# Performance work log

Hardware: AMD Instinct MI355X
Metric: run time of the kernel (lower is better)

Reference implementation:

```python
import jax, jax.numpy as jnp
import numpy as np

B, T, D, H, Q = 8, 1024, 256, 4, 3
DK = D // H


def _ln(x, g, b):
    m = x.mean(-1, keepdims=True)
    v = x.var(-1, keepdims=True)
    return (x - m) / jnp.sqrt(v + 1e-5) * g + b


def _grn(x, f1w, f1b, f2w, f2b, gw, gb, lng, lnb):
    # GatedResidualNetwork (input_size == output_size, dropout in eval mode)
    eta1 = jax.nn.elu(x @ f1w.T + f1b)
    eta2 = eta1 @ f2w.T + f2b
    a = jax.nn.sigmoid(eta2 @ gw.T + gb) * eta2
    return _ln(x + a, lng, lnb)


def setup_inputs() -> dict:
    key = jax.random.key(0)
    ks = jax.random.split(key, 24)
    s = 0.02
    p = {}
    p['x'] = jax.random.normal(ks[0], (B, T, D), dtype=jnp.float32)
    # GRN 1 (temporal enrichment before attention)
    p['g1_f1w'] = jax.random.normal(ks[1], (D, D)) * s
    p['g1_f1b'] = jnp.zeros((D,))
    p['g1_f2w'] = jax.random.normal(ks[2], (D, D)) * s
    p['g1_f2b'] = jnp.zeros((D,))
    p['g1_gw'] = jax.random.normal(ks[3], (D, D)) * s
    p['g1_gb'] = jnp.zeros((D,))
    p['g1_lng'] = jnp.ones((D,))
    p['g1_lnb'] = jnp.zeros((D,))
    # Multi-head self-attention
    p['wq'] = jax.random.normal(ks[4], (D, D)) * s
    p['wk'] = jax.random.normal(ks[5], (D, D)) * s
    p['wv'] = jax.random.normal(ks[6], (D, D)) * s
    p['wo_w'] = jax.random.normal(ks[7], (D, D)) * s
    p['wo_b'] = jnp.zeros((D,))
    p['attn_lng'] = jnp.ones((D,))
    p['attn_lnb'] = jnp.zeros((D,))
    # GRN 2 (post-attention gating)
    p['g2_f1w'] = jax.random.normal(ks[8], (D, D)) * s
    p['g2_f1b'] = jnp.zeros((D,))
    p['g2_f2w'] = jax.random.normal(ks[9], (D, D)) * s
    p['g2_f2b'] = jnp.zeros((D,))
    p['g2_gw'] = jax.random.normal(ks[10], (D, D)) * s
    p['g2_gb'] = jnp.zeros((D,))
    p['g2_lng'] = jnp.ones((D,))
    p['g2_lnb'] = jnp.zeros((D,))
    # Quantile heads: Linear(D -> Q)
    p['qh_w'] = jax.random.normal(ks[11], (Q, D)) * s
    p['qh_b'] = jnp.zeros((Q,))
    return p


def reference(x, g1_f1w, g1_f1b, g1_f2w, g1_f2b, g1_gw, g1_gb, g1_lng, g1_lnb,
              wq, wk, wv, wo_w, wo_b, attn_lng, attn_lnb,
              g2_f1w, g2_f1b, g2_f2w, g2_f2b, g2_gw, g2_gb, g2_lng, g2_lnb,
              qh_w, qh_b):
    b, t, d = x.shape
    h = _grn(x, g1_f1w, g1_f1b, g1_f2w, g1_f2b, g1_gw, g1_gb, g1_lng, g1_lnb)
    # self-attention (W_q/W_k/W_v have no bias, per module)
    q = (h @ wq.T).reshape(b, t, H, DK)
    k = (h @ wk.T).reshape(b, t, H, DK)
    v = (h @ wv.T).reshape(b, t, H, DK)
    scale = 1.0 / np.sqrt(DK).astype(np.float32)
    scores = jnp.einsum('bthd,bshd->bhts', q, k) * scale  # [B,H,T,T]
    attn = jax.nn.softmax(scores, axis=-1)
    ctx = jnp.einsum('bhts,bshd->bthd', attn, v).reshape(b, t, d)
    attn_out = ctx @ wo_w.T + wo_b
    h2 = _ln(h + attn_out, attn_lng, attn_lnb)
    h3 = _grn(h2, g2_f1w, g2_f1b, g2_f2w, g2_f2b, g2_gw, g2_gb, g2_lng, g2_lnb)
    # quantile heads on the last decoder step (CUDAQuantileHeadsFunction: [B,D]->[B,Q])
    out = h3[:, -1, :] @ qh_w.T + qh_b  # [B, Q]
    return out
```

## Files before the change

kernel.cpp:

```cpp
#include <hip/hip_runtime.h>
#include <hip/hip_bf16.h>
#include <math.h>

#define DD 256
#define BB 8
#define TT 1024
#define MM (BB*TT)
#define NH 4
#define DKH 64
#define NQ 3
#define SPLIT 16
#define SROWS (TT/SPLIT)

typedef __attribute__((ext_vector_type(8))) short bf16x8;
typedef __attribute__((ext_vector_type(4))) float f32x4;
typedef unsigned short u16;
typedef unsigned int u32;

__device__ __forceinline__ float bf2f(u16 u) {
  return __uint_as_float(((u32)u) << 16);
}
__device__ __forceinline__ u16 f2bf(float x) {
  __hip_bfloat16 h = __float2bfloat16(x);
  return *reinterpret_cast<u16*>(&h);
}
__device__ __forceinline__ uint2 pack4(float a, float b, float c, float d) {
  uint2 r;
  r.x = (u32)f2bf(a) | ((u32)f2bf(b) << 16);
  r.y = (u32)f2bf(c) | ((u32)f2bf(d) << 16);
  return r;
}
__device__ __forceinline__ float wred(float v) {
#pragma unroll
  for (int off = 32; off; off >>= 1) v += __shfl_xor(v, off);
  return v;
}

template<bool ABF, int ACT>
__global__ __launch_bounds__(256) void gemm64(const void* __restrict__ A_,
                                              const float* __restrict__ W,
                                              const float* __restrict__ bias,
                                              u16* __restrict__ out)
{
  __shared__ u16 As[64][264];
  __shared__ u16 Bs[64][264];
  const int tid  = threadIdx.x;
  const int lane = tid & 63, wave = tid >> 6;
  const int wr = wave >> 1, wc = wave & 1;
  const int q  = lane >> 4, lr = lane & 15;
  const int m0 = blockIdx.x * 64, n0 = blockIdx.y * 64;

#pragma unroll
  for (int p = 0; p < 8; ++p) {
    const int c = tid + p * 256;
    const int row = c >> 5, col = (c & 31) * 8;
    if constexpr (ABF) {
      *(uint4*)&As[row][col] = *(const uint4*)((const u16*)A_ + (size_t)(m0 + row) * DD + col);
    } else {
      const float* ap = (const float*)A_ + (size_t)(m0 + row) * DD + col;
      const float4 v0 = *(const float4*)ap, v1 = *(const float4*)(ap + 4);
      *(uint2*)&As[row][col]     = pack4(v0.x, v0.y, v0.z, v0.w);
      *(uint2*)&As[row][col + 4] = pack4(v1.x, v1.y, v1.z, v1.w);
    }
    const float* wp = W + (size_t)(n0 + row) * DD + col;
    const float4 w0 = *(const float4*)wp, w1 = *(const float4*)(wp + 4);
    *(uint2*)&Bs[row][col]     = pack4(w0.x, w0.y, w0.z, w0.w);
    *(uint2*)&Bs[row][col + 4] = pack4(w1.x, w1.y, w1.z, w1.w);
  }
  __syncthreads();

  f32x4 acc[2][2] = {};
#pragma unroll
  for (int kk = 0; kk < 8; ++kk) {
    const int koff = kk * 32 + q * 8;
    bf16x8 av[2], bv[2];
    av[0] = *(const bf16x8*)&As[wr * 32 + lr][koff];
    av[1] = *(const bf16x8*)&As[wr * 32 + 16 + lr][koff];
    bv[0] = *(const bf16x8*)&Bs[wc * 32 + lr][koff];
    bv[1] = *(const bf16x8*)&Bs[wc * 32 + 16 + lr][koff];
#pragma unroll
    for (int i = 0; i < 2; ++i)
#pragma unroll
      for (int j = 0; j < 2; ++j)
        acc[i][j] = __builtin_amdgcn_mfma_f32_16x16x32_bf16(av[i], bv[j], acc[i][j], 0, 0, 0);
  }

#pragma unroll
  for (int i = 0; i < 2; ++i) {
#pragma unroll
    for (int j = 0; j < 2; ++j) {
      const int col = n0 + wc * 32 + j * 16 + lr;
      const float bvv = bias ? bias[col] : 0.f;
#pragma unroll
      for (int t = 0; t < 4; ++t) {
        const int row = m0 + wr * 32 + i * 16 + q * 4 + t;
        float v = acc[i][j][t] + bvv;
        if (ACT == 1) v = v > 0.f ? v : expm1f(v);
        out[(size_t)row * DD + col] = f2bf(v);
      }
    }
  }
}

__global__ __launch_bounds__(256) void grn_gate_ln(
    const u16* __restrict__ eta2, const float* __restrict__ W,
    const float* __restrict__ gb, const float* __restrict__ x,
    const float* __restrict__ lng, const float* __restrict__ lnb,
    u16* __restrict__ hout, float* __restrict__ hlast)
{
  __shared__ u16 As[32][136];
  __shared__ u16 Bs[256][136];
  __shared__ float red_s[32][5];
  __shared__ float red_q[32][5];
  __shared__ float smean[32], srstd[32];

  const int tid  = threadIdx.x;
  const int lane = tid & 63, wave = tid >> 6;
  const int q  = lane >> 4, lr = lane & 15;
  const int m0 = blockIdx.x * 32;

  f32x4 acc[2][4] = {};

  for (int k0 = 0; k0 < DD; k0 += 128) {
#pragma unroll
    for (int p = 0; p < 2; ++p) {
      const int c = tid + p * 256;
      const int row = c >> 4, col = (c & 15) * 8;
      *(uint4*)&As[row][col] = *(const uint4*)(eta2 + (size_t)(m0 + row) * DD + k0 + col);
    }
#pragma unroll
    for (int p = 0; p < 16; ++p) {
      const int c = tid + p * 256;
      const int row = c >> 4, col = (c & 15) * 8;
      const float* wp = W + (size_t)row * DD + k0 + col;
      const float4 w0 = *(const float4*)wp, w1 = *(const float4*)(wp + 4);
      *(uint2*)&Bs[row][col]     = pack4(w0.x, w0.y, w0.z, w0.w);
      *(uint2*)&Bs[row][col + 4] = pack4(w1.x, w1.y, w1.z, w1.w);
    }
    __syncthreads();
#pragma unroll
    for (int kk = 0; kk < 4; ++kk) {
      const int koff = kk * 32 + q * 8;
      bf16x8 av[2], bv[4];
#pragma unroll
      for (int i = 0; i < 2; ++i) av[i] = *(const bf16x8*)&As[i * 16 + lr][koff];
#pragma unroll
      for (int j = 0; j < 4; ++j) bv[j] = *(const bf16x8*)&Bs[wave * 64 + j * 16 + lr][koff];
#pragma unroll
      for (int i = 0; i < 2; ++i)
#pragma unroll
        for (int j = 0; j < 4; ++j)
          acc[i][j] = __builtin_amdgcn_mfma_f32_16x16x32_bf16(av[i], bv[j], acc[i][j], 0, 0, 0);
    }
    __syncthreads();
  }

  float pre[2][4][4];
#pragma unroll
  for (int i = 0; i < 2; ++i) {
#pragma unroll
    for (int j = 0; j < 4; ++j) {
      const int n = wave * 64 + j * 16 + lr;
      const float gbn = gb[n];
#pragma unroll
      for (int t = 0; t < 4; ++t) {
        const int grow = m0 + i * 16 + q * 4 + t;
        const float gate = acc[i][j][t] + gbn;
        const float sig = 1.f / (1.f + expf(-gate));
        const float e2 = bf2f(eta2[(size_t)grow * DD + n]);
        pre[i][j][t] = x[(size_t)grow * DD + n] + sig * e2;
      }
    }
  }
#pragma unroll
  for (int i = 0; i < 2; ++i) {
#pragma unroll
    for (int t = 0; t < 4; ++t) {
      float s = 0.f, sq = 0.f;
#pragma unroll
      for (int j = 0; j < 4; ++j) { const float v = pre[i][j][t]; s += v; sq += v * v; }
#pragma unroll
      for (int m = 1; m <= 8; m <<= 1) { s += __shfl_xor(s, m); sq += __shfl_xor(sq, m); }
      if (lr == 0) {
        const int ml = i * 16 + q * 4 + t;
        red_s[ml][wave] = s;
        red_q[ml][wave] = sq;
      }
    }
  }
  __syncthreads();
  if (tid < 32) {
    const float s  = red_s[tid][0] + red_s[tid][1] + red_s[tid][2] + red_s[tid][3];
    const float sq = red_q[tid][0] + red_q[tid][1] + red_q[tid][2] + red_q[tid][3];
    const float mean = s * (1.f / DD);
    const float var = sq * (1.f / DD) - mean * mean;
    smean[tid] = mean;
    srstd[tid] = rsqrtf(var + 1e-5f);
  }
  __syncthreads();
#pragma unroll
  for (int i = 0; i < 2; ++i) {
#pragma unroll
    for (int j = 0; j < 4; ++j) {
      const int n = wave * 64 + j * 16 + lr;
      const float gn = lng[n], bn = lnb[n];
#pragma unroll
      for (int t = 0; t < 4; ++t) {
        const int ml = i * 16 + q * 4 + t;
        const int grow = m0 + ml;
        const float hn = (pre[i][j][t] - smean[ml]) * srstd[ml] * gn + bn;
        hout[(size_t)grow * DD + n] = f2bf(hn);
        if ((grow & (TT - 1)) == (TT - 1))
          hlast[(size_t)(grow >> 10) * DD + n] = hn;
      }
    }
  }
}

__global__ __launch_bounds__(256) void attn_partial(
    const float* __restrict__ hlast, const u16* __restrict__ hbuf,
    const float* __restrict__ wq, const float* __restrict__ wk,
    const float* __restrict__ wo_w, const float* __restrict__ f1w,
    const float* __restrict__ f2w, const float* __restrict__ gw,
    const float* __restrict__ wv,
    u16* __restrict__ wbf,
    float* __restrict__ p_eh,
    float* __restrict__ p_den)
{
  __shared__ float hl[DD];
  __shared__ float qv[DD];
  __shared__ float qk[NH][DD];
  __shared__ float ehp[4][NH][DD];
  __shared__ float denp[4][NH];
  const int chunk = blockIdx.x, b = blockIdx.y;
  const int tid = threadIdx.x, lane = tid & 63, w = tid >> 6;
  const int l32 = lane & 31, half = lane >> 5;

  {
    const int bid = b * SPLIT + chunk;
    const int base = bid * 2560;
#pragma unroll
    for (int r = 0; r < 10; ++r) {
      const int e = base + r * 256 + tid;
      const int mi = e >> 16, off = e & 65535;
      const float* s = (mi == 0) ? wo_w : (mi == 1) ? f1w : (mi == 2) ? f2w
                     : (mi == 3) ? gw : wv;
      wbf[e] = f2bf(s[off]);
    }
  }

  if (tid < DD) hl[tid] = hlast[(size_t)b * DD + tid];
  __syncthreads();

  {
    float sv[8];
    const float4 s0 = *(const float4*)(hl + l32 * 8);
    const float4 s1 = *(const float4*)(hl + l32 * 8 + 4);
    sv[0] = s0.x; sv[1] = s0.y; sv[2] = s0.z; sv[3] = s0.w;
    sv[4] = s1.x; sv[5] = s1.y; sv[6] = s1.z; sv[7] = s1.w;
#pragma unroll
    for (int i = 0; i < 32; ++i) {
      const int r = w * 64 + i * 2 + half;
      const float* wr_ = wq + (size_t)r * DD + l32 * 8;
      const float4 w0 = *(const float4*)wr_;
      const float4 w1 = *(const float4*)(wr_ + 4);
      float acc = w0.x * sv[0] + w0.y * sv[1] + w0.z * sv[2] + w0.w * sv[3]
                + w1.x * sv[4] + w1.y * sv[5] + w1.z * sv[6] + w1.w * sv[7];
#pragma unroll
      for (int off = 16; off; off >>= 1) acc += __shfl_xor(acc, off);
      if (l32 == 0) qv[r] = acc;
    }
  }
  __syncthreads();

  {
    float acc[4] = {};
    for (int d = 0; d < 64; ++d) {
      const int r = w * 64 + d;
      const float qd = qv[r];
      const float4 kv = *(const float4*)(wk + (size_t)r * DD + lane * 4);
      acc[0] += qd * kv.x; acc[1] += qd * kv.y;
      acc[2] += qd * kv.z; acc[3] += qd * kv.w;
    }
#pragma unroll
    for (int i = 0; i < 4; ++i) qk[w][lane * 4 + i] = acc[i] * 0.125f;
  }
  __syncthreads();

  {
    float qkr[NH][4];
#pragma unroll
    for (int h = 0; h < NH; ++h) {
      const float4 qq = *(const float4*)&qk[h][lane * 4];
      qkr[h][0] = qq.x; qkr[h][1] = qq.y; qkr[h][2] = qq.z; qkr[h][3] = qq.w;
    }
    float ehacc[NH][4] = {};
    float dacc[NH] = {};
    const int sbase = chunk * SROWS + w * 16;
    for (int ii = 0; ii < 16; ++ii) {
      const int s = sbase + ii;
      const uint2 hv2 = *(const uint2*)(hbuf + ((size_t)(b * TT + s)) * DD + lane * 4);
      float hv[4];
      hv[0] = bf2f((u16)(hv2.x & 0xffffu)); hv[1] = bf2f((u16)(hv2.x >> 16));
      hv[2] = bf2f((u16)(hv2.y & 0xffffu)); hv[3] = bf2f((u16)(hv2.y >> 16));
      float sc[NH];
#pragma unroll
      for (int h = 0; h < NH; ++h) {
        float p = qkr[h][0] * hv[0] + qkr[h][1] * hv[1]
                + qkr[h][2] * hv[2] + qkr[h][3] * hv[3];
        sc[h] = wred(p);
      }
#pragma unroll
      for (int h = 0; h < NH; ++h) {
        const float E = __expf(fminf(fmaxf(sc[h], -30.f), 30.f));
        dacc[h] += E;
        ehacc[h][0] += E * hv[0]; ehacc[h][1] += E * hv[1];
        ehacc[h][2] += E * hv[2]; ehacc[h][3] += E * hv[3];
      }
    }
#pragma unroll
    for (int h = 0; h < NH; ++h) {
      *(float4*)&ehp[w][h][lane * 4] =
          make_float4(ehacc[h][0], ehacc[h][1], ehacc[h][2], ehacc[h][3]);
      if (lane == 0) denp[w][h] = dacc[h];
    }
  }
  __syncthreads();

  {
    const size_t pb = ((size_t)(b * SPLIT + chunk)) * NH * DD;
#pragma unroll
    for (int h = 0; h < NH; ++h)
      p_eh[pb + h * DD + tid] =
          ehp[0][h][tid] + ehp[1][h][tid] + ehp[2][h][tid] + ehp[3][h][tid];
    if (tid < NH)
      p_den[(b * SPLIT + chunk) * NH + tid] =
          denp[0][tid] + denp[1][tid] + denp[2][tid] + denp[3][tid];
  }
}

__device__ __forceinline__ void mv256b(const u16* __restrict__ W16,
                                       const float* __restrict__ srcbuf,
                                       float* __restrict__ dst,
                                       int wave, int lane)
{
  const int half = lane >> 5, l32 = lane & 31;
  float s[8];
  {
    const float4 s0 = *(const float4*)(srcbuf + l32 * 8);
    const float4 s1 = *(const float4*)(srcbuf + l32 * 8 + 4);
    s[0] = s0.x; s[1] = s0.y; s[2] = s0.z; s[3] = s0.w;
    s[4] = s1.x; s[5] = s1.y; s[6] = s1.z; s[7] = s1.w;
  }
#pragma unroll
  for (int i = 0; i < 8; ++i) {
    const int r = wave * 16 + i * 2 + half;
    const bf16x8 wv = *(const bf16x8*)(W16 + (size_t)r * DD + l32 * 8);
    float acc = 0.f;
#pragma unroll
    for (int e = 0; e < 8; ++e) acc += bf2f((u16)wv[e]) * s[e];
#pragma unroll
    for (int off = 16; off; off >>= 1) acc += __shfl_xor(acc, off);
    if (l32 == 0) dst[r] = acc;
  }
}

#define LN_STEP(val, gam, bet, dst) \
  __syncthreads(); \
  if (tid < DD) { lnS[tid] = (val); lnQ[tid] = (val) * (val); } \
  __syncthreads(); \
  if (tid < 64) { \
    float s_ = 0.f, q_ = 0.f; \
    _Pragma("unroll") \
    for (int i_ = 0; i_ < 4; ++i_) { s_ += lnS[tid + 64 * i_]; q_ += lnQ[tid + 64 * i_]; } \
    s_ = wred(s_); q_ = wred(q_); \
    if (tid == 0) { const float m_ = s_ * (1.f / DD); red2[0] = m_; red2[1] = rsqrtf(q_ * (1.f / DD) - m_ * m_ + 1e-5f); } \
  } \
  __syncthreads(); \
  if (tid < DD) dst[tid] = ((val) - red2[0]) * red2[1] * gam[tid] + bet[tid]; \
  __syncthreads();

__global__ __launch_bounds__(1024) void tail3(
    const float* __restrict__ hlast, const float* __restrict__ p_eh,
    const float* __restrict__ p_den, const u16* __restrict__ wbf,
    const float* __restrict__ wob, const float* __restrict__ alng, const float* __restrict__ alnb,
    const float* __restrict__ f1b, const float* __restrict__ f2b,
    const float* __restrict__ gbv, const float* __restrict__ lng, const float* __restrict__ lnb,
    const float* __restrict__ qhw, const float* __restrict__ qhb,
    float* __restrict__ out)
{
  __shared__ float pv[NH * DD];
  __shared__ float den[NH];
  __shared__ float hl[DD], bufA[DD], bufB[DD], bufC[DD], part0[DD];
  __shared__ float lnS[DD], lnQ[DD];
  __shared__ float red2[2];
  const int b = blockIdx.x, tid = threadIdx.x;
  const int wave = tid >> 6, lane = tid & 63;
  const int half = lane >> 5, l32 = lane & 31;

  float ehsum = 0.f;
  for (int c = 0; c < SPLIT; ++c)
    ehsum += p_eh[((size_t)(b * SPLIT + c)) * NH * DD + tid];
  if (tid < NH) {
    float s = 0.f;
    for (int c = 0; c < SPLIT; ++c) s += p_den[(b * SPLIT + c) * NH + tid];
    den[tid] = s;
  }
  if (tid < DD) hl[tid] = hlast[(size_t)b * DD + tid];
  __syncthreads();
  pv[tid] = ehsum / den[tid >> 8];
  __syncthreads();

  {
    const u16* wv16 = wbf + 4 * 65536;
#pragma unroll
    for (int i = 0; i < 8; ++i) {
      const int r = wave * 16 + i * 2 + half;
      const float* sp = pv + (r >> 6) * DD + l32 * 8;
      const float4 s0 = *(const float4*)sp;
      const float4 s1 = *(const float4*)(sp + 4);
      const bf16x8 wvv = *(const bf16x8*)(wv16 + (size_t)r * DD + l32 * 8);
      float acc = bf2f((u16)wvv[0]) * s0.x + bf2f((u16)wvv[1]) * s0.y
                + bf2f((u16)wvv[2]) * s0.z + bf2f((u16)wvv[3]) * s0.w
                + bf2f((u16)wvv[4]) * s1.x + bf2f((u16)wvv[5]) * s1.y
                + bf2f((u16)wvv[6]) * s1.z + bf2f((u16)wvv[7]) * s1.w;
#pragma unroll
      for (int off = 16; off; off >>= 1) acc += __shfl_xor(acc, off);
      if (l32 == 0) bufB[r] = acc;
    }
  }
  __syncthreads();

  mv256b(wbf + 0 * 65536, bufB, part0, wave, lane);
  __syncthreads();
  float v = 0.f;
  if (tid < DD) v = hl[tid] + part0[tid] + wob[tid];
  LN_STEP(v, alng, alnb, bufA)

  mv256b(wbf + 1 * 65536, bufA, part0, wave, lane);
  __syncthreads();
  if (tid < DD) {
    const float e1 = part0[tid] + f1b[tid];
    bufB[tid] = e1 > 0.f ? e1 : expm1f(e1);
  }
  __syncthreads();

  mv256b(wbf + 2 * 65536, bufB, part0, wave, lane);
  __syncthreads();
  if (tid < DD) bufC[tid] = part0[tid] + f2b[tid];
  __syncthreads();

  mv256b(wbf + 3 * 65536, bufC, part0, wave, lane);
  __syncthreads();
  v = 0.f;
  if (tid < DD) {
    const float g = part0[tid] + gbv[tid];
    v = bufA[tid] + (1.f / (1.f + expf(-g))) * bufC[tid];
  }
  LN_STEP(v, lng, lnb, bufA)

  if (tid < 64 * NQ) {
    const int qi = tid >> 6, l = tid & 63;
    float acc = 0.f;
#pragma unroll
    for (int i = 0; i < 4; ++i) acc += qhw[(size_t)qi * DD + l + 64 * i] * bufA[l + 64 * i];
    acc = wred(acc);
    if (l == 0) out[b * NQ + qi] = acc + qhb[qi];
  }
}

extern "C" void kernel_launch(void* const* d_in, const int* in_sizes, int n_in,
                              void* d_out, int out_size, void* d_ws, size_t ws_size,
                              hipStream_t stream)
{
  const float* x       = (const float*)d_in[0];
  const float* g1_f1w  = (const float*)d_in[1];
  const float* g1_f1b  = (const float*)d_in[2];
  const float* g1_f2w  = (const float*)d_in[3];
  const float* g1_f2b  = (const float*)d_in[4];
  const float* g1_gw   = (const float*)d_in[5];
  const float* g1_gb   = (const float*)d_in[6];
  const float* g1_lng  = (const float*)d_in[7];
  const float* g1_lnb  = (const float*)d_in[8];
  const float* wq      = (const float*)d_in[9];
  const float* wk      = (const float*)d_in[10];
  const float* wv      = (const float*)d_in[11];
  const float* wo_w    = (const float*)d_in[12];
  const float* wo_b    = (const float*)d_in[13];
  const float* attn_lng= (const float*)d_in[14];
  const float* attn_lnb= (const float*)d_in[15];
  const float* g2_f1w  = (const float*)d_in[16];
  const float* g2_f1b  = (const float*)d_in[17];
  const float* g2_f2w  = (const float*)d_in[18];
  const float* g2_f2b  = (const float*)d_in[19];
  const float* g2_gw   = (const float*)d_in[20];
  const float* g2_gb   = (const float*)d_in[21];
  const float* g2_lng  = (const float*)d_in[22];
  const float* g2_lnb  = (const float*)d_in[23];
  const float* qh_w    = (const float*)d_in[24];
  const float* qh_b    = (const float*)d_in[25];
  float* out = (float*)d_out;

  char* w8 = (char*)d_ws;
  u16*  wbf   = (u16*)(w8);
  float* p_eh  = (float*)(w8 + ((size_t)1 << 20));
  float* p_den = (float*)(w8 + ((size_t)1600 << 10));
  u16*  eta1  = (u16*)(w8 + ((size_t)2  << 20));
  u16*  eta2  = (u16*)(w8 + ((size_t)6  << 20));
  u16*  hbuf  = (u16*)(w8 + ((size_t)10 << 20));
  float* hlast = (float*)(w8 + ((size_t)14 << 20));

  const dim3 blk(256);
  const dim3 g1(MM / 64, DD / 64);

  gemm64<false, 1><<<g1, blk, 0, stream>>>((const void*)x,    g1_f1w, g1_f1b, eta1);
  gemm64<true,  0><<<g1, blk, 0, stream>>>((const void*)eta1, g1_f2w, g1_f2b, eta2);
  grn_gate_ln<<<dim3(MM / 32), blk, 0, stream>>>(eta2, g1_gw, g1_gb, x, g1_lng, g1_lnb, hbuf, hlast);
  attn_partial<<<dim3(SPLIT, BB), blk, 0, stream>>>(hlast, hbuf, wq, wk,
                                                    wo_w, g2_f1w, g2_f2w, g2_gw, wv,
                                                    wbf, p_eh, p_den);
  tail3<<<dim3(BB), dim3(1024), 0, stream>>>(hlast, p_eh, p_den, wbf,
                                             wo_b, attn_lng, attn_lnb,
                                             g2_f1b, g2_f2b, g2_gb, g2_lng, g2_lnb,
                                             qh_w, qh_b, out);
}
```

Baseline: 89.60 us.

## Rewrite attention partial kernel with LDS-staged rows and doubled key split

Doubles the key-dimension split so twice as many blocks each handle 32 rows. Each block now stages its rows of h in LDS and computes per-row scores with 8 threads per row and short shuffles, where before it did a full-wave reduction per row and head. It then accumulates the E-weighted sums per column thread. The q and qk projections are re-partitioned across threads, and workspace offsets are shifted to fit the larger partial buffers. The tail kernel must now reduce twice as many partials, and each block still recomputes the wq/wk matvecs redundantly.

Result: faster. 82.02 us (-8.5%).

```diff
diff --git a/kernel.cpp b/kernel.cpp
--- a/kernel.cpp
+++ b/kernel.cpp
@@ -9,7 +9,7 @@
 #define NH 4
 #define DKH 64
 #define NQ 3
-#define SPLIT 16
+#define SPLIT 32
 #define SROWS (TT/SPLIT)
 
 typedef __attribute__((ext_vector_type(8))) short bf16x8;
@@ -217,7 +217,7 @@
   }
 }
 
-__global__ __launch_bounds__(256) void attn_partial(
+__global__ __launch_bounds__(256) void attn2(
     const float* __restrict__ hlast, const u16* __restrict__ hbuf,
     const float* __restrict__ wq, const float* __restrict__ wk,
     const float* __restrict__ wo_w, const float* __restrict__ f1w,
@@ -229,18 +229,17 @@
 {
   __shared__ float hl[DD];
   __shared__ float qv[DD];
-  __shared__ float qk[NH][DD];
-  __shared__ float ehp[4][NH][DD];
-  __shared__ float denp[4][NH];
+  __shared__ float qk4[NH][DD];
+  __shared__ u16 hch[SROWS][264];
+  __shared__ float E[SROWS][NH];
   const int chunk = blockIdx.x, b = blockIdx.y;
-  const int tid = threadIdx.x, lane = tid & 63, w = tid >> 6;
-  const int l32 = lane & 31, half = lane >> 5;
+  const int tid = threadIdx.x;
 
   {
     const int bid = b * SPLIT + chunk;
-    const int base = bid * 2560;
-#pragma unroll
-    for (int r = 0; r < 10; ++r) {
+    const int base = bid * 1280;
+#pragma unroll
+    for (int r = 0; r < 5; ++r) {
       const int e = base + r * 256 + tid;
       const int mi = e >> 16, off = e & 65535;
       const float* s = (mi == 0) ? wo_w : (mi == 1) ? f1w : (mi == 2) ? f2w
@@ -249,93 +248,93 @@
     }
   }
 
-  if (tid < DD) hl[tid] = hlast[(size_t)b * DD + tid];
-  __syncthreads();
-
-  {
-    float sv[8];
-    const float4 s0 = *(const float4*)(hl + l32 * 8);
-    const float4 s1 = *(const float4*)(hl + l32 * 8 + 4);
-    sv[0] = s0.x; sv[1] = s0.y; sv[2] = s0.z; sv[3] = s0.w;
-    sv[4] = s1.x; sv[5] = s1.y; sv[6] = s1.z; sv[7] = s1.w;
-#pragma unroll
-    for (int i = 0; i < 32; ++i) {
-      const int r = w * 64 + i * 2 + half;
-      const float* wr_ = wq + (size_t)r * DD + l32 * 8;
-      const float4 w0 = *(const float4*)wr_;
-      const float4 w1 = *(const float4*)(wr_ + 4);
-      float acc = w0.x * sv[0] + w0.y * sv[1] + w0.z * sv[2] + w0.w * sv[3]
-                + w1.x * sv[4] + w1.y * sv[5] + w1.z * sv[6] + w1.w * sv[7];
-#pragma unroll
-      for (int off = 16; off; off >>= 1) acc += __shfl_xor(acc, off);
-      if (l32 == 0) qv[r] = acc;
-    }
-  }
-  __syncthreads();
-
-  {
-    float acc[4] = {};
-    for (int d = 0; d < 64; ++d) {
-      const int r = w * 64 + d;
-      const float qd = qv[r];
-      const float4 kv = *(const float4*)(wk + (size_t)r * DD + lane * 4);
-      acc[0] += qd * kv.x; acc[1] += qd * kv.y;
-      acc[2] += qd * kv.z; acc[3] += qd * kv.w;
-    }
-#pragma unroll
-    for (int i = 0; i < 4; ++i) qk[w][lane * 4 + i] = acc[i] * 0.125f;
-  }
-  __syncthreads();
-
-  {
-    float qkr[NH][4];
+  hl[tid] = hlast[(size_t)b * DD + tid];
+#pragma unroll
+  for (int p = 0; p < 4; ++p) {
+    const int idx = p * 256 + tid;
+    const int row = idx >> 5, col = (idx & 31) * 8;
+    *(uint4*)&hch[row][col] =
+        *(const uint4*)(hbuf + ((size_t)(b * TT + chunk * SROWS + row)) * DD + col);
+  }
+  __syncthreads();
+
+  {
+    const int j = tid >> 2, seg = tid & 3;
+    const float* sp = hl + seg * 64;
+#pragma unroll
+    for (int pass = 0; pass < 4; ++pass) {
+      const int r = pass * 64 + j;
+      const float* wr_ = wq + (size_t)r * DD + seg * 64;
+      float acc = 0.f;
+#pragma unroll
+      for (int k = 0; k < 64; k += 4) {
+        const float4 w4 = *(const float4*)(wr_ + k);
+        acc += w4.x * sp[k] + w4.y * sp[k + 1] + w4.z * sp[k + 2] + w4.w * sp[k + 3];
+      }
+      acc += __shfl_xor(acc, 1);
+      acc += __shfl_xor(acc, 2);
+      if (seg == 0) qv[r] = acc;
+    }
+  }
+  __syncthreads();
+
+  {
 #pragma unroll
     for (int h = 0; h < NH; ++h) {
-      const float4 qq = *(const float4*)&qk[h][lane * 4];
-      qkr[h][0] = qq.x; qkr[h][1] = qq.y; qkr[h][2] = qq.z; qkr[h][3] = qq.w;
-    }
-    float ehacc[NH][4] = {};
-    float dacc[NH] = {};
-    const int sbase = chunk * SROWS + w * 16;
-    for (int ii = 0; ii < 16; ++ii) {
-      const int s = sbase + ii;
-      const uint2 hv2 = *(const uint2*)(hbuf + ((size_t)(b * TT + s)) * DD + lane * 4);
-      float hv[4];
-      hv[0] = bf2f((u16)(hv2.x & 0xffffu)); hv[1] = bf2f((u16)(hv2.x >> 16));
-      hv[2] = bf2f((u16)(hv2.y & 0xffffu)); hv[3] = bf2f((u16)(hv2.y >> 16));
-      float sc[NH];
+      float acc = 0.f;
+      const float* wkb = wk + (size_t)(h * DKH) * DD + tid;
+#pragma unroll 8
+      for (int d = 0; d < DKH; ++d)
+        acc += qv[h * DKH + d] * wkb[(size_t)d * DD];
+      qk4[h][tid] = acc * 0.125f;
+    }
+  }
+  __syncthreads();
+
+  {
+    const int s = tid >> 3, sub = tid & 7;
+    const u16* hp = &hch[s][sub * 32];
+    float part[NH] = {};
+#pragma unroll
+    for (int v = 0; v < 4; ++v) {
+      const bf16x8 h8 = *(const bf16x8*)(hp + v * 8);
+      float hf[8];
+#pragma unroll
+      for (int e = 0; e < 8; ++e) hf[e] = bf2f((u16)h8[e]);
 #pragma unroll
       for (int h = 0; h < NH; ++h) {
-        float p = qkr[h][0] * hv[0] + qkr[h][1] * hv[1]
-                + qkr[h][2] * hv[2] + qkr[h][3] * hv[3];
-        sc[h] = wred(p);
+        const float* qp = &qk4[h][sub * 32 + v * 8];
+#pragma unroll
+        for (int e = 0; e < 8; ++e) part[h] += hf[e] * qp[e];
       }
-#pragma unroll
-      for (int h = 0; h < NH; ++h) {
-        const float E = __expf(fminf(fmaxf(sc[h], -30.f), 30.f));
-        dacc[h] += E;
-        ehacc[h][0] += E * hv[0]; ehacc[h][1] += E * hv[1];
-        ehacc[h][2] += E * hv[2]; ehacc[h][3] += E * hv[3];
-      }
     }
 #pragma unroll
     for (int h = 0; h < NH; ++h) {
-      *(float4*)&ehp[w][h][lane * 4] =
-          make_float4(ehacc[h][0], ehacc[h][1], ehacc[h][2], ehacc[h][3]);
-      if (lane == 0) denp[w][h] = dacc[h];
-    }
-  }
-  __syncthreads();
-
-  {
+      float p = part[h];
+      p += __shfl_xor(p, 1);
+      p += __shfl_xor(p, 2);
+      p += __shfl_xor(p, 4);
+      if (sub == 0) E[s][h] = __expf(fminf(fmaxf(p, -30.f), 30.f));
+    }
+  }
+  __syncthreads();
+
+  {
+    float eh[NH] = {};
+    for (int s = 0; s < SROWS; ++s) {
+      const float hv = bf2f(hch[s][tid]);
+      const float4 E4 = *(const float4*)&E[s][0];
+      eh[0] += E4.x * hv; eh[1] += E4.y * hv;
+      eh[2] += E4.z * hv; eh[3] += E4.w * hv;
+    }
     const size_t pb = ((size_t)(b * SPLIT + chunk)) * NH * DD;
 #pragma unroll
-    for (int h = 0; h < NH; ++h)
-      p_eh[pb + h * DD + tid] =
-          ehp[0][h][tid] + ehp[1][h][tid] + ehp[2][h][tid] + ehp[3][h][tid];
-    if (tid < NH)
-      p_den[(b * SPLIT + chunk) * NH + tid] =
-          denp[0][tid] + denp[1][tid] + denp[2][tid] + denp[3][tid];
+    for (int h = 0; h < NH; ++h) p_eh[pb + h * DD + tid] = eh[h];
+  }
+  if (tid < NH) {
+    float s = 0.f;
+    for (int s2 = 0; s2 < SROWS; ++s2) s += E[s2][tid];
+    p_den[(b * SPLIT + chunk) * NH + tid] = s;
   }
 }
 
@@ -504,11 +503,11 @@
   char* w8 = (char*)d_ws;
   u16*  wbf   = (u16*)(w8);
   float* p_eh  = (float*)(w8 + ((size_t)1 << 20));
-  float* p_den = (float*)(w8 + ((size_t)1600 << 10));
-  u16*  eta1  = (u16*)(w8 + ((size_t)2  << 20));
-  u16*  eta2  = (u16*)(w8 + ((size_t)6  << 20));
-  u16*  hbuf  = (u16*)(w8 + ((size_t)10 << 20));
-  float* hlast = (float*)(w8 + ((size_t)14 << 20));
+  float* p_den = (float*)(w8 + ((size_t)2100 << 10));
+  u16*  eta1  = (u16*)(w8 + ((size_t)4  << 20));
+  u16*  eta2  = (u16*)(w8 + ((size_t)8  << 20));
+  u16*  hbuf  = (u16*)(w8 + ((size_t)12 << 20));
+  float* hlast = (float*)(w8 + ((size_t)16 << 20));
 
   const dim3 blk(256);
   const dim3 g1(MM / 64, DD / 64);
@@ -516,9 +515,9 @@
   gemm64<false, 1><<<g1, blk, 0, stream>>>((const void*)x,    g1_f1w, g1_f1b, eta1);
   gemm64<true,  0><<<g1, blk, 0, stream>>>((const void*)eta1, g1_f2w, g1_f2b, eta2);
   grn_gate_ln<<<dim3(MM / 32), blk, 0, stream>>>(eta2, g1_gw, g1_gb, x, g1_lng, g1_lnb, hbuf, hlast);
-  attn_partial<<<dim3(SPLIT, BB), blk, 0, stream>>>(hlast, hbuf, wq, wk,
-                                                    wo_w, g2_f1w, g2_f2w, g2_gw, wv,
-                                                    wbf, p_eh, p_den);
+  attn2<<<dim3(SPLIT, BB), blk, 0, stream>>>(hlast, hbuf, wq, wk,
+                                             wo_w, g2_f1w, g2_f2w, g2_gw, wv,
+                                             wbf, p_eh, p_den);
   tail3<<<dim3(BB), dim3(1024), 0, stream>>>(hlast, p_eh, p_den, wbf,
                                              wo_b, attn_lng, attn_lnb,
                                              g2_f1b, g2_f2b, g2_gb, g2_lng, g2_lnb,
```
